# Performance work log

Measured on AMD Instinct MI355X. Metric: run time of the kernel, lower is better.

Reference implementation:

```python
import jax, jax.numpy as jnp
import numpy as np

NUM_USER = 100000
NUM_ITEM = 50000
DIM = 64
NUM_EDGES = 3200000


def setup_inputs() -> dict:
    key = jax.random.key(0)
    k1, k2, k3, k4 = jax.random.split(key, 4)
    return {
        "user_embedding": jax.random.normal(k1, (NUM_USER, DIM), dtype=jnp.float32),
        "item_embedding": jax.random.normal(k2, (NUM_ITEM, DIM), dtype=jnp.float32),
        "edge_user": jax.random.randint(k3, (NUM_EDGES,), 0, NUM_USER, dtype=jnp.int32).astype(jnp.int64),
        "edge_item": jax.random.randint(k4, (NUM_EDGES,), 0, NUM_ITEM, dtype=jnp.int32).astype(jnp.int64),
    }


def _segment_mean(feats, idx, num_segments):
    # scatter_mean semantics: sum per segment / count, empty segments -> 0
    s = jax.ops.segment_sum(feats, idx, num_segments=num_segments)  # [n, dim]
    cnt = jax.ops.segment_sum(jnp.ones((idx.shape[0], 1), feats.dtype), idx,
                              num_segments=num_segments)  # [n, 1]
    return s / jnp.maximum(cnt, 1.0)


def reference(user_embedding, item_embedding, edge_user, edge_item):
    num_user = user_embedding.shape[0]
    num_item = item_embedding.shape[0]

    # view1: aggregate_neighbor_features — mean of purchased-item embeddings per user
    neighbor_feat = _segment_mean(item_embedding[edge_item], edge_user, num_user)

    # view2: aggregate_cooccurrence_features — two-stage mean aggregation
    # stage 1: per item, mean of its purchasers' embeddings
    item_user_agg = _segment_mean(user_embedding[edge_user], edge_item, num_item)
    # stage 2: per user, mean of stage-1 features of purchased items
    cooccur_feat = _segment_mean(item_user_agg[edge_item], edge_user, num_user)

    return (neighbor_feat, cooccur_feat)
```

## Files before the change

### kernel.cpp

```cpp
#include <hip/hip_runtime.h>
#include <hip/hip_fp16.h>

constexpr int NUM_USER  = 100000;
constexpr int NUM_ITEM  = 50000;
constexpr int DIM       = 64;
constexpr int NUM_EDGES = 3200000;

constexpr int KPB   = 32;
constexpr int NB_U  = (NUM_USER + KPB - 1) / KPB;
constexpr int NB_I  = (NUM_ITEM + KPB - 1) / KPB;
constexpr int CHUNK = 4096;
constexpr int CSH   = 14;
constexpr int NCH_I = 4;
constexpr int NCH_U = 7;
constexpr int CAP_U = 1280;
constexpr int CAP_I = 2304;
constexpr int PGRID = 256;
constexpr int CVTB  = 256;
constexpr int NG    = 196;
constexpr int GSH_U = 9;
constexpr int GSH_I = 8;
constexpr int FBG_U = 16;
constexpr int FBG_I = 8;
constexpr int GCAP  = 17152;

__device__ __forceinline__ __half2 u2h(unsigned u) {
  union { unsigned u; __half2 h; } v; v.u = u; return v.h;
}
__device__ __forceinline__ unsigned h2u(__half2 h) {
  union { __half2 h; unsigned u; } v; v.h = h; return v.u;
}
__device__ __forceinline__ float u_as_f(unsigned u) {
  union { unsigned u; float f; } v; v.u = u; return v.f;
}

__device__ __forceinline__ int detect64(const void* eu, const void* ei) {
  const int* a = (const int*)eu;
  const int* b = (const int*)ei;
  int any = 0;
#pragma unroll
  for (int i = 1; i < 64; i += 2) { any |= a[i]; any |= b[i]; }
  return any == 0;
}

__device__ __forceinline__ int idx_at(const void* p, int e, int is64) {
  return is64 ? ((const int*)p)[2 * e] : ((const int*)p)[e];
}

__device__ __forceinline__ void cvt_body(int t0, int stride,
                                         const float* __restrict__ ue,
                                         unsigned* __restrict__ u32,
                                         const float* __restrict__ ie,
                                         unsigned* __restrict__ fused) {
  const int nu = NUM_USER * 32, ni = NUM_ITEM * 32;
  for (int t = t0; t < nu + ni; t += stride) {
    if (t < nu) {
      const unsigned long long raw =
          __builtin_nontemporal_load((const unsigned long long*)ue + t);
      const __half2 h = __floats2half2_rn(u_as_f((unsigned)raw),
                                          u_as_f((unsigned)(raw >> 32)));
      __builtin_nontemporal_store(h2u(h), &u32[t]);
    } else {
      const int s = t - nu;
      const unsigned long long raw =
          __builtin_nontemporal_load((const unsigned long long*)ie + s);
      const __half2 h = __floats2half2_rn(u_as_f((unsigned)raw),
                                          u_as_f((unsigned)(raw >> 32)));
      __builtin_nontemporal_store(h2u(h),
                                  &fused[(size_t)(s >> 5) * 64 + 2 * (s & 31)]);
    }
  }
}

__global__ void k_passA(const void* eu_p, const void* ei_p,
                        int* gccur_u, int* gccur_i,
                        unsigned* __restrict__ coarse_u,
                        unsigned* __restrict__ coarse_i,
                        const float* __restrict__ ue, unsigned* __restrict__ u32t,
                        const float* __restrict__ ie, unsigned* __restrict__ fusedt) {
  __shared__ int hu[NG], bu[NG];
  __shared__ int hi_[NG], bi_[NG];
  if (blockIdx.x >= PGRID) {
    cvt_body((blockIdx.x - PGRID) * blockDim.x + threadIdx.x,
             CVTB * blockDim.x, ue, u32t, ie, fusedt);
    return;
  }
  for (int t = threadIdx.x; t < NG; t += blockDim.x) { hu[t] = 0; hi_[t] = 0; }
  __syncthreads();
  const int is64 = detect64(eu_p, ei_p);
  const int ch = NUM_EDGES / PGRID;
  const int lo = blockIdx.x * ch, hiE = lo + ch;
  for (int e = lo + threadIdx.x; e < hiE; e += blockDim.x) {
    atomicAdd(&hu[idx_at(eu_p, e, is64) >> GSH_U], 1);
    atomicAdd(&hi_[idx_at(ei_p, e, is64) >> GSH_I], 1);
  }
  __syncthreads();
  for (int t = threadIdx.x; t < NG; t += blockDim.x) {
    const int h0 = hu[t];
    bu[t] = h0 ? atomicAdd(&gccur_u[t], h0) : 0;
    hu[t] = 0;
    const int h1 = hi_[t];
    bi_[t] = h1 ? atomicAdd(&gccur_i[t], h1) : 0;
    hi_[t] = 0;
  }
  __syncthreads();
  for (int e = lo + threadIdx.x; e < hiE; e += blockDim.x) {
    const int eu = idx_at(eu_p, e, is64);
    const int ei = idx_at(ei_p, e, is64);
    const int gu = eu >> GSH_U;
    const int pu = bu[gu] + atomicAdd(&hu[gu], 1);
    if (pu < GCAP)
      coarse_u[(size_t)gu * GCAP + pu] =
          ((unsigned)(eu & ((1 << GSH_U) - 1)) << 17) | (unsigned)ei;
    const int gi = ei >> GSH_I;
    const int pi = bi_[gi] + atomicAdd(&hi_[gi], 1);
    if (pi < GCAP)
      coarse_i[(size_t)gi * GCAP + pi] =
          ((unsigned)(ei & ((1 << GSH_I) - 1)) << 17) | (unsigned)eu;
  }
}

__global__ void k_passB(const unsigned* __restrict__ coarse_u,
                        const unsigned* __restrict__ coarse_i,
                        const int* __restrict__ gccur_u,
                        const int* __restrict__ gccur_i,
                        unsigned* __restrict__ pairs_u,
                        unsigned* __restrict__ pairs_i,
                        int* __restrict__ gcnt_u, int* __restrict__ gcnt_i) {
  __shared__ int h[FBG_U], cur[FBG_U];
  const bool isU = blockIdx.x < NG;
  const int g = isU ? blockIdx.x : blockIdx.x - NG;
  const unsigned* src = (isU ? coarse_u : coarse_i) + (size_t)g * GCAP;
  int n = isU ? gccur_u[g] : gccur_i[g];
  n = min(n, GCAP);
  const int FB = isU ? FBG_U : FBG_I;
  const int CAP = isU ? CAP_U : CAP_I;
  const int NBfin = isU ? NB_U : NB_I;
  unsigned* dst = isU ? pairs_u : pairs_i;
  int* gcnt = isU ? gcnt_u : gcnt_i;
  const int tid = threadIdx.x;

  if (tid < FB) h[tid] = 0;
  __syncthreads();
  for (int j = tid; j < n; j += blockDim.x)
    atomicAdd(&h[(src[j] >> 22) & (FB - 1)], 1);
  __syncthreads();
  if (tid < FB) {
    const int fbg = g * FB + tid;
    if (fbg < NBfin) gcnt[fbg] = min(h[tid], CAP);
    cur[tid] = 0;
  }
  __syncthreads();
  for (int j = tid; j < n; j += blockDim.x) {
    const unsigned p = src[j];
    const int fb = (p >> 22) & (FB - 1);
    const int pos = atomicAdd(&cur[fb], 1);
    if (pos < CAP)
      dst[(size_t)(g * FB + fb) * CAP + pos] = p & 0x3FFFFFu;
  }
}

__global__ void k_part2cvt(const void* eu_p, const void* ei_p,
                           int* gcur_i, unsigned int* __restrict__ pairs_i,
                           int* gcur_u, unsigned int* __restrict__ pairs_u,
                           const float* __restrict__ ue, unsigned* __restrict__ u32t,
                           const float* __restrict__ ie, unsigned* __restrict__ fusedt) {
  __shared__ int hist_u[NB_U], base_u[NB_U];
  __shared__ int hist_i[NB_I], base_i[NB_I];
  if (blockIdx.x >= PGRID) {
    cvt_body((blockIdx.x - PGRID) * blockDim.x + threadIdx.x,
             CVTB * blockDim.x, ue, u32t, ie, fusedt);
    return;
  }
  for (int t = threadIdx.x; t < NB_U; t += blockDim.x) hist_u[t] = 0;
  for (int t = threadIdx.x; t < NB_I; t += blockDim.x) hist_i[t] = 0;
  __syncthreads();
  const int is64 = detect64(eu_p, ei_p);
  const int ch = NUM_EDGES / PGRID;
  const int lo = blockIdx.x * ch, hiE = lo + ch;
  for (int e = lo + threadIdx.x; e < hiE; e += blockDim.x) {
    atomicAdd(&hist_u[idx_at(eu_p, e, is64) >> 5], 1);
    atomicAdd(&hist_i[idx_at(ei_p, e, is64) >> 5], 1);
  }
  __syncthreads();
  for (int t = threadIdx.x; t < NB_U; t += blockDim.x) {
    const int h = hist_u[t];
    base_u[t] = h ? t * CAP_U + atomicAdd(&gcur_u[t], h) : 0;
    hist_u[t] = 0;
  }
  for (int t = threadIdx.x; t < NB_I; t += blockDim.x) {
    const int h = hist_i[t];
    base_i[t] = h ? t * CAP_I + atomicAdd(&gcur_i[t], h) : 0;
    hist_i[t] = 0;
  }
  __syncthreads();
  for (int e = lo + threadIdx.x; e < hiE; e += blockDim.x) {
    const int eu = idx_at(eu_p, e, is64);
    const int ei = idx_at(ei_p, e, is64);
    const int bi = ei >> 5;
    const int pi = base_i[bi] + atomicAdd(&hist_i[bi], 1);
    if (pi < (bi + 1) * CAP_I)
      pairs_i[pi] = ((unsigned)(ei & 31) << 17) | (unsigned)eu;
    const int bu = eu >> 5;
    const int pu = base_u[bu] + atomicAdd(&hist_u[bu], 1);
    if (pu < (bu + 1) * CAP_U)
      pairs_u[pu] = ((unsigned)(eu & 31) << 17) | (unsigned)ei;
  }
}

__global__ __launch_bounds__(256, 8)
void k_agg_item(const unsigned* __restrict__ user32,
                const unsigned int* __restrict__ pairs,
                const int* __restrict__ gcnt,
                unsigned* __restrict__ fused) {
  constexpr int NBINS = NCH_U * KPB;
  __shared__ int sorted[CHUNK];
  __shared__ int hist[NBINS], base[NBINS], cur[NBINS];
  __shared__ int gsum[NCH_U];
  const int tid = threadIdx.x;
  const int lane = tid & 63;
  const int wid = tid >> 6;
  const int half = lane >> 5;
  const int c = lane & 31;
  const int bucket = blockIdx.x;
  const int lo = bucket * CAP_I;
  const int hi = lo + min(gcnt[bucket], CAP_I);

  unsigned s[8]; int cnt[8];
#pragma unroll
  for (int r = 0; r < 8; ++r) { s[r] = 0u; cnt[r] = 0; }

  for (int clo = lo; clo < hi; clo += CHUNK) {
    const int csz = min(CHUNK, hi - clo);
    for (int t = tid; t < NBINS; t += 256) hist[t] = 0;
    __syncthreads();
    for (int j = tid; j < csz; j += 256) {
      const unsigned p = pairs[clo + j];
      atomicAdd(&hist[((p & 0x1FFFF) >> CSH) * KPB + (p >> 17)], 1);
    }
    __syncthreads();
    if (tid < NCH_U) {
      int g = 0;
      for (int q = 0; q < KPB; ++q) g += hist[tid * KPB + q];
      gsum[tid] = g;
    }
    __syncthreads();
    for (int t = tid; t < NBINS; t += 256) {
      const int ch = t >> 5;
      int b = 0;
      for (int q = 0; q < ch; ++q) b += gsum[q];
      for (int q = ch * KPB; q < t; ++q) b += hist[q];
      base[t] = b; cur[t] = b;
    }
    __syncthreads();
    for (int j = tid; j < csz; j += 256) {
      const unsigned p = pairs[clo + j];
      const int v = (int)(p & 0x1FFFF);
      const int slot = atomicAdd(&cur[(v >> CSH) * KPB + (p >> 17)], 1);
      sorted[slot] = v;
    }
    __syncthreads();
    for (int ch = 0; ch < NCH_U; ++ch) {
#pragma unroll
      for (int r = 0; r < 8; ++r) {
        const int bin = ch * KPB + wid * 8 + r;
        const int jlo = base[bin], jhi = cur[bin];
        cnt[r] += jhi - jlo;
        for (int j = jlo; j < jhi; j += 8) {
          unsigned w[4];
#pragma unroll
          for (int q = 0; q < 4; ++q) {
            const int jj = j + 2 * q + half;
            w[q] = (jj < jhi) ? user32[(size_t)sorted[jj] * 32 + c] : 0u;
          }
#pragma unroll
          for (int q = 0; q < 4; ++q)
            s[r] = h2u(__hadd2(u2h(s[r]), u2h(w[q])));
        }
      }
    }
    __syncthreads();
  }

  const int i0 = bucket * KPB;
#pragma unroll
  for (int r = 0; r < 8; ++r) {
    const unsigned o = (unsigned)__shfl_xor((int)s[r], 32);
    const __half2 tot = __hadd2(u2h(s[r]), u2h(o));
    const int item = i0 + wid * 8 + r;
    if (half == 0 && item < NUM_ITEM) {
      const float inv = 1.0f / fmaxf((float)cnt[r], 1.f);
      fused[(size_t)item * 64 + 2 * c + 1] =
          h2u(__floats2half2_rn(__low2float(tot) * inv, __high2float(tot) * inv));
    }
  }
}

__global__ __launch_bounds__(256, 8)
void k_agg_user(const unsigned* __restrict__ fused,
                const unsigned int* __restrict__ pairs,
                const int* __restrict__ gcnt,
                float* __restrict__ out0, float* __restrict__ out1) {
  constexpr int NBINS = NCH_I * KPB;
  __shared__ int sorted[CHUNK];
  __shared__ int hist[NBINS], base[NBINS], cur[NBINS];
  __shared__ int gsum[NCH_I];
  const int tid = threadIdx.x;
  const int lane = tid & 63;
  const int wid = tid >> 6;
  const int half = lane >> 5;
  const int c = lane & 31;
  const int bucket = blockIdx.x;
  const int lo = bucket * CAP_U;
  const int hi = lo + min(gcnt[bucket], CAP_U);
  const uint2* fused2 = (const uint2*)fused;

  unsigned s0[8], s1[8]; int cnt[8];
#pragma unroll
  for (int r = 0; r < 8; ++r) { s0[r] = 0u; s1[r] = 0u; cnt[r] = 0; }

  for (int clo = lo; clo < hi; clo += CHUNK) {
    const int csz = min(CHUNK, hi - clo);
    for (int t = tid; t < NBINS; t += 256) hist[t] = 0;
    __syncthreads();
    for (int j = tid; j < csz; j += 256) {
      const unsigned p = pairs[clo + j];
      atomicAdd(&hist[((p & 0x1FFFF) >> CSH) * KPB + (p >> 17)], 1);
    }
    __syncthreads();
    if (tid < NCH_I) {
      int g = 0;
      for (int q = 0; q < KPB; ++q) g += hist[tid * KPB + q];
      gsum[tid] = g;
    }
    __syncthreads();
    for (int t = tid; t < NBINS; t += 256) {
      const int ch = t >> 5;
      int b = 0;
      for (int q = 0; q < ch; ++q) b += gsum[q];
      for (int q = ch * KPB; q < t; ++q) b += hist[q];
      base[t] = b; cur[t] = b;
    }
    __syncthreads();
    for (int j = tid; j < csz; j += 256) {
      const unsigned p = pairs[clo + j];
      const int v = (int)(p & 0x1FFFF);
      const int slot = atomicAdd(&cur[(v >> CSH) * KPB + (p >> 17)], 1);
      sorted[slot] = v;
    }
    __syncthreads();
    for (int ch = 0; ch < NCH_I; ++ch) {
#pragma unroll
      for (int r = 0; r < 8; ++r) {
        const int bin = ch * KPB + wid * 8 + r;
        const int jlo = base[bin], jhi = cur[bin];
        cnt[r] += jhi - jlo;
        for (int j = jlo; j < jhi; j += 8) {
          uint2 w[4];
#pragma unroll
          for (int q = 0; q < 4; ++q) {
            const int jj = j + 2 * q + half;
            w[q] = (jj < jhi) ? fused2[(size_t)sorted[jj] * 32 + c]
                              : make_uint2(0u, 0u);
          }
#pragma unroll
          for (int q = 0; q < 4; ++q) {
            s0[r] = h2u(__hadd2(u2h(s0[r]), u2h(w[q].x)));
            s1[r] = h2u(__hadd2(u2h(s1[r]), u2h(w[q].y)));
          }
        }
      }
    }
    __syncthreads();
  }

  const int u0 = bucket * KPB;
#pragma unroll
  for (int r = 0; r < 8; ++r) {
    const unsigned o0 = (unsigned)__shfl_xor((int)s0[r], 32);
    const unsigned o1 = (unsigned)__shfl_xor((int)s1[r], 32);
    const __half2 t0 = __hadd2(u2h(s0[r]), u2h(o0));
    const __half2 t1 = __hadd2(u2h(s1[r]), u2h(o1));
    const int u = u0 + wid * 8 + r;
    if (half == 0 && u < NUM_USER) {
      const float inv = 1.0f / fmaxf((float)cnt[r], 1.f);
      ((float2*)out0)[(size_t)u * 32 + c] =
          make_float2(__low2float(t0) * inv, __high2float(t0) * inv);
      ((float2*)out1)[(size_t)u * 32 + c] =
          make_float2(__low2float(t1) * inv, __high2float(t1) * inv);
    }
  }
}

__global__ void k_scatter1(const float* __restrict__ user_emb,
                           const float* __restrict__ item_emb,
                           const void* eu_p, const void* ei_p,
                           float* out0, float* item_sum,
                           float* cnt_user, float* cnt_item) {
  const int is64 = detect64(eu_p, ei_p);
  const int lane = threadIdx.x & (DIM - 1);
  const int sub  = threadIdx.x >> 6;
  const int epb  = blockDim.x >> 6;
  for (int e = blockIdx.x * epb + sub; e < NUM_EDGES; e += gridDim.x * epb) {
    const int eu = idx_at(eu_p, e, is64);
    const int ei = idx_at(ei_p, e, is64);
    atomicAdd(&out0[eu * DIM + lane], item_emb[ei * DIM + lane]);
    atomicAdd(&item_sum[ei * DIM + lane], user_emb[eu * DIM + lane]);
    if (lane == 0) {
      atomicAdd(&cnt_user[eu], 1.0f);
      atomicAdd(&cnt_item[ei], 1.0f);
    }
  }
}

__global__ void k_div_item(float* item_sum, const float* __restrict__ cnt_item) {
  const int n = NUM_ITEM * DIM;
  for (int t = blockIdx.x * blockDim.x + threadIdx.x; t < n;
       t += gridDim.x * blockDim.x)
    item_sum[t] /= fmaxf(cnt_item[t >> 6], 1.0f);
}

__global__ void k_scatter2(const float* __restrict__ item_agg,
                           const void* eu_p, const void* ei_p, float* out1) {
  const int is64 = detect64(eu_p, ei_p);
  const int lane = threadIdx.x & (DIM - 1);
  const int sub  = threadIdx.x >> 6;
  const int epb  = blockDim.x >> 6;
  for (int e = blockIdx.x * epb + sub; e < NUM_EDGES; e += gridDim.x * epb) {
    const int eu = idx_at(eu_p, e, is64);
    const int ei = idx_at(ei_p, e, is64);
    atomicAdd(&out1[eu * DIM + lane], item_agg[ei * DIM + lane]);
  }
}

__global__ void k_finalize(float* out0, float* out1,
                           const float* __restrict__ cnt_user) {
  const int n = NUM_USER * DIM;
  for (int t = blockIdx.x * blockDim.x + threadIdx.x; t < n;
       t += gridDim.x * blockDim.x) {
    const float c = fmaxf(cnt_user[t >> 6], 1.0f);
    out0[t] /= c;
    out1[t] /= c;
  }
}

extern "C" void kernel_launch(void* const* d_in, const int* in_sizes, int n_in,
                              void* d_out, int out_size, void* d_ws, size_t ws_size,
                              hipStream_t stream) {
  const float* user_emb = (const float*)d_in[0];
  const float* item_emb = (const float*)d_in[1];
  const void*  eu_p     = d_in[2];
  const void*  ei_p     = d_in[3];

  float* out0 = (float*)d_out;
  float* out1 = out0 + (size_t)NUM_USER * DIM;

  int* wsi = (int*)d_ws;
  float* wsf = (float*)d_ws;

  const size_t t0_coarse_u = 0;
  const size_t t0_coarse_i = t0_coarse_u + (size_t)NG * GCAP;
  const size_t t0_pairs_u  = t0_coarse_i + (size_t)NG * GCAP;
  const size_t t0_pairs_i  = t0_pairs_u + (size_t)NB_U * CAP_U;
  const size_t t0_user32   = t0_pairs_i + (size_t)NB_I * CAP_I;
  const size_t t0_fused    = t0_user32 + (size_t)NUM_USER * 32;
  const size_t t0_gccur    = t0_fused + (size_t)NUM_ITEM * 64;
  const size_t t0_gcnt_u   = t0_gccur + 2 * NG;
  const size_t t0_gcnt_i   = t0_gcnt_u + NB_U;
  const size_t need_t0     = (t0_gcnt_i + NB_I) * 4;

  const size_t s_pairs_u = 0;
  const size_t s_pairs_i = s_pairs_u + (size_t)NB_U * CAP_U;
  const size_t s_user32  = s_pairs_i + (size_t)NB_I * CAP_I;
  const size_t s_fused   = s_user32 + (size_t)NUM_USER * 32;
  const size_t s_gcur_u  = s_fused + (size_t)NUM_ITEM * 64;
  const size_t s_gcur_i  = s_gcur_u + NB_U;
  const size_t need_t1   = (s_gcur_i + NB_I) * 4;

  if (ws_size >= need_t0) {
    unsigned* coarse_u = (unsigned*)(wsi + t0_coarse_u);
    unsigned* coarse_i = (unsigned*)(wsi + t0_coarse_i);
    unsigned* pairs_u  = (unsigned*)(wsi + t0_pairs_u);
    unsigned* pairs_i  = (unsigned*)(wsi + t0_pairs_i);
    unsigned* user32   = (unsigned*)(wsi + t0_user32);
    unsigned* fused    = (unsigned*)(wsi + t0_fused);
    int* gccur_u = wsi + t0_gccur;
    int* gccur_i = gccur_u + NG;
    int* gcnt_u  = wsi + t0_gcnt_u;
    int* gcnt_i  = wsi + t0_gcnt_i;

    hipMemsetAsync(gccur_u, 0, (size_t)(2 * NG) * 4, stream);
    k_passA<<<PGRID + CVTB, 1024, 0, stream>>>(eu_p, ei_p, gccur_u, gccur_i,
                                               coarse_u, coarse_i,
                                               user_emb, user32, item_emb, fused);
    k_passB<<<2 * NG, 1024, 0, stream>>>(coarse_u, coarse_i, gccur_u, gccur_i,
                                         pairs_u, pairs_i, gcnt_u, gcnt_i);
    k_agg_item<<<NB_I, 256, 0, stream>>>(user32, pairs_i, gcnt_i, fused);
    k_agg_user<<<NB_U, 256, 0, stream>>>(fused, pairs_u, gcnt_u, out0, out1);
  } else if (ws_size >= need_t1) {
    unsigned* pairs_u = (unsigned*)(wsi + s_pairs_u);
    unsigned* pairs_i = (unsigned*)(wsi + s_pairs_i);
    unsigned* user32  = (unsigned*)(wsi + s_user32);
    unsigned* fused   = (unsigned*)(wsi + s_fused);
    int* gcur_u = wsi + s_gcur_u;
    int* gcur_i = wsi + s_gcur_i;

    hipMemsetAsync(gcur_u, 0, (size_t)(NB_U + NB_I) * 4, stream);
    k_part2cvt<<<PGRID + CVTB, 1024, 0, stream>>>(eu_p, ei_p, gcur_i, pairs_i,
                                                  gcur_u, pairs_u,
                                                  user_emb, user32,
                                                  item_emb, fused);
    k_agg_item<<<NB_I, 256, 0, stream>>>(user32, pairs_i, gcur_i, fused);
    k_agg_user<<<NB_U, 256, 0, stream>>>(fused, pairs_u, gcur_u, out0, out1);
  } else {
    float* item_sum = wsf;
    float* cnt_user = wsf + (size_t)NUM_ITEM * DIM;
    float* cnt_item = cnt_user + NUM_USER;
    const size_t used = ((size_t)NUM_ITEM * DIM + NUM_USER + NUM_ITEM) * 4;

    hipMemsetAsync(d_out, 0, (size_t)out_size * sizeof(float), stream);
    hipMemsetAsync(d_ws, 0, used, stream);
    k_scatter1<<<4096, 256, 0, stream>>>(user_emb, item_emb, eu_p, ei_p,
                                         out0, item_sum, cnt_user, cnt_item);
    k_div_item<<<2048, 256, 0, stream>>>(item_sum, cnt_item);
    k_scatter2<<<4096, 256, 0, stream>>>(item_sum, eu_p, ei_p, out1);
    k_finalize<<<2048, 256, 0, stream>>>(out0, out1, cnt_user);
  }
}
```

Baseline: 227.8 us.

## Sort pairs by fine bin in passB and drop per-block re-sort in aggregators

passB now builds a full histogram over (fine bucket, chunk, key) bins, computes exclusive prefix offsets, writes pairs in fully sorted order, and stores per-bin offsets as 16-bit arrays in workspace. New aggregation kernels read these offsets into shared memory and walk the pre-sorted pairs directly, skipping the per-block shared-memory histogram, scan and scatter. The cost is larger shared histograms and more scan work in passB, plus extra workspace for the offset tables. The aggregators also lose their large shared arrays, which may allow more blocks per CU.

```diff
diff --git a/kernel.cpp b/kernel.cpp
--- a/kernel.cpp
+++ b/kernel.cpp
@@ -13,6 +13,8 @@
 constexpr int CSH   = 14;
 constexpr int NCH_I = 4;
 constexpr int NCH_U = 7;
+constexpr int BPB_U = NCH_I * KPB;
+constexpr int BPB_I = NCH_U * KPB;
 constexpr int CAP_U = 1280;
 constexpr int CAP_I = 2304;
 constexpr int PGRID = 256;
@@ -126,37 +128,205 @@
                         const int* __restrict__ gccur_i,
                         unsigned* __restrict__ pairs_u,
                         unsigned* __restrict__ pairs_i,
-                        int* __restrict__ gcnt_u, int* __restrict__ gcnt_i) {
-  __shared__ int h[FBG_U], cur[FBG_U];
+                        int* __restrict__ gcnt_u, int* __restrict__ gcnt_i,
+                        unsigned short* __restrict__ boff_u,
+                        unsigned short* __restrict__ boff_i) {
+  __shared__ int hist[FBG_U * BPB_U];
+  __shared__ int base[FBG_U * BPB_U];
+  __shared__ int ssum[FBG_U * (BPB_I / 16)];
+  __shared__ int totl[FBG_U];
   const bool isU = blockIdx.x < NG;
   const int g = isU ? blockIdx.x : blockIdx.x - NG;
   const unsigned* src = (isU ? coarse_u : coarse_i) + (size_t)g * GCAP;
   int n = isU ? gccur_u[g] : gccur_i[g];
   n = min(n, GCAP);
   const int FB = isU ? FBG_U : FBG_I;
+  const int BPB = isU ? BPB_U : BPB_I;
+  const int SEC = BPB >> 4;
   const int CAP = isU ? CAP_U : CAP_I;
   const int NBfin = isU ? NB_U : NB_I;
   unsigned* dst = isU ? pairs_u : pairs_i;
   int* gcnt = isU ? gcnt_u : gcnt_i;
+  unsigned short* boff = isU ? boff_u : boff_i;
+  const int nbins = FB * BPB;
   const int tid = threadIdx.x;
 
-  if (tid < FB) h[tid] = 0;
-  __syncthreads();
-  for (int j = tid; j < n; j += blockDim.x)
-    atomicAdd(&h[(src[j] >> 22) & (FB - 1)], 1);
-  __syncthreads();
-  if (tid < FB) {
-    const int fbg = g * FB + tid;
-    if (fbg < NBfin) gcnt[fbg] = min(h[tid], CAP);
-    cur[tid] = 0;
-  }
+  for (int t = tid; t < nbins; t += blockDim.x) hist[t] = 0;
   __syncthreads();
   for (int j = tid; j < n; j += blockDim.x) {
     const unsigned p = src[j];
-    const int fb = (p >> 22) & (FB - 1);
-    const int pos = atomicAdd(&cur[fb], 1);
+    const int lk = (int)(p >> 17);
+    const int v = (int)(p & 0x1FFFF);
+    atomicAdd(&hist[(lk >> 5) * BPB + (v >> CSH) * KPB + (lk & 31)], 1);
+  }
+  __syncthreads();
+  for (int s = tid; s < FB * SEC; s += blockDim.x) {
+    int acc = 0;
+    const int b0 = s * 16;
+#pragma unroll
+    for (int q = 0; q < 16; ++q) acc += hist[b0 + q];
+    ssum[s] = acc;
+  }
+  __syncthreads();
+  if (tid < FB) {
+    int run = 0;
+    for (int q = 0; q < SEC; ++q) {
+      const int t = ssum[tid * SEC + q];
+      ssum[tid * SEC + q] = run;
+      run += t;
+    }
+    totl[tid] = run;
+  }
+  __syncthreads();
+  for (int b = tid; b < nbins; b += blockDim.x) {
+    const int fb = b / BPB;
+    const int w = b - fb * BPB;
+    const int sec = w >> 4;
+    int acc = ssum[fb * SEC + sec];
+    const int b0 = fb * BPB + (sec << 4);
+    for (int q = b0; q < b; ++q) acc += hist[q];
+    base[b] = acc;
+  }
+  __syncthreads();
+  for (int b = tid; b < nbins; b += blockDim.x) {
+    const int fb = b / BPB;
+    const int fbg = g * FB + fb;
+    if (fbg < NBfin) {
+      const int w = b - fb * BPB;
+      boff[(size_t)fbg * (BPB + 1) + w] = (unsigned short)min(base[b], CAP);
+      if (w == 0) {
+        boff[(size_t)fbg * (BPB + 1) + BPB] = (unsigned short)min(totl[fb], CAP);
+        gcnt[fbg] = min(totl[fb], CAP);
+      }
+    }
+  }
+  __syncthreads();
+  for (int j = tid; j < n; j += blockDim.x) {
+    const unsigned p = src[j];
+    const int lk = (int)(p >> 17);
+    const int v = (int)(p & 0x1FFFF);
+    const int fb = lk >> 5;
+    const int pos = atomicAdd(&base[fb * BPB + (v >> CSH) * KPB + (lk & 31)], 1);
     if (pos < CAP)
-      dst[(size_t)(g * FB + fb) * CAP + pos] = p & 0x3FFFFFu;
+      dst[(size_t)(g * FB + fb) * CAP + pos] = (unsigned)v;
+  }
+}
+
+__global__ __launch_bounds__(256, 8)
+void k_agg_item_f(const unsigned* __restrict__ user32,
+                  const unsigned* __restrict__ pairs,
+                  const unsigned short* __restrict__ boff,
+                  unsigned* __restrict__ fused) {
+  __shared__ unsigned short off[BPB_I + 1];
+  const int tid = threadIdx.x;
+  const int lane = tid & 63;
+  const int wid = tid >> 6;
+  const int half = lane >> 5;
+  const int c = lane & 31;
+  const int bucket = blockIdx.x;
+  for (int t = tid; t < BPB_I + 1; t += 256)
+    off[t] = boff[(size_t)bucket * (BPB_I + 1) + t];
+  __syncthreads();
+  const size_t pbase = (size_t)bucket * CAP_I;
+
+  unsigned s[8]; int cnt[8];
+#pragma unroll
+  for (int r = 0; r < 8; ++r) { s[r] = 0u; cnt[r] = 0; }
+
+  for (int ch = 0; ch < NCH_U; ++ch) {
+#pragma unroll
+    for (int r = 0; r < 8; ++r) {
+      const int bin = ch * KPB + wid * 8 + r;
+      const int jlo = off[bin], jhi = off[bin + 1];
+      cnt[r] += jhi - jlo;
+      for (int j = jlo; j < jhi; j += 8) {
+        unsigned w[4];
+#pragma unroll
+        for (int q = 0; q < 4; ++q) {
+          const int jj = j + 2 * q + half;
+          w[q] = (jj < jhi) ? user32[(size_t)pairs[pbase + jj] * 32 + c] : 0u;
+        }
+#pragma unroll
+        for (int q = 0; q < 4; ++q)
+          s[r] = h2u(__hadd2(u2h(s[r]), u2h(w[q])));
+      }
+    }
+  }
+
+  const int i0 = bucket * KPB;
+#pragma unroll
+  for (int r = 0; r < 8; ++r) {
+    const unsigned o = (unsigned)__shfl_xor((int)s[r], 32);
+    const __half2 tot = __hadd2(u2h(s[r]), u2h(o));
+    const int item = i0 + wid * 8 + r;
+    if (half == 0 && item < NUM_ITEM) {
+      const float inv = 1.0f / fmaxf((float)cnt[r], 1.f);
+      fused[(size_t)item * 64 + 2 * c + 1] =
+          h2u(__floats2half2_rn(__low2float(tot) * inv, __high2float(tot) * inv));
+    }
+  }
+}
+
+__global__ __launch_bounds__(256, 8)
+void k_agg_user_f(const unsigned* __restrict__ fused,
+                  const unsigned* __restrict__ pairs,
+                  const unsigned short* __restrict__ boff,
+                  float* __restrict__ out0, float* __restrict__ out1) {
+  __shared__ unsigned short off[BPB_U + 1];
+  const int tid = threadIdx.x;
+  const int lane = tid & 63;
+  const int wid = tid >> 6;
+  const int half = lane >> 5;
+  const int c = lane & 31;
+  const int bucket = blockIdx.x;
+  for (int t = tid; t < BPB_U + 1; t += 256)
+    off[t] = boff[(size_t)bucket * (BPB_U + 1) + t];
+  __syncthreads();
+  const size_t pbase = (size_t)bucket * CAP_U;
+  const uint2* fused2 = (const uint2*)fused;
+
+  unsigned s0[8], s1[8]; int cnt[8];
+#pragma unroll
+  for (int r = 0; r < 8; ++r) { s0[r] = 0u; s1[r] = 0u; cnt[r] = 0; }
+
+  for (int ch = 0; ch < NCH_I; ++ch) {
+#pragma unroll
+    for (int r = 0; r < 8; ++r) {
+      const int bin = ch * KPB + wid * 8 + r;
+      const int jlo = off[bin], jhi = off[bin + 1];
+      cnt[r] += jhi - jlo;
+      for (int j = jlo; j < jhi; j += 8) {
+        uint2 w[4];
+#pragma unroll
+        for (int q = 0; q < 4; ++q) {
+          const int jj = j + 2 * q + half;
+          w[q] = (jj < jhi) ? fused2[(size_t)pairs[pbase + jj] * 32 + c]
+                            : make_uint2(0u, 0u);
+        }
+#pragma unroll
+        for (int q = 0; q < 4; ++q) {
+          s0[r] = h2u(__hadd2(u2h(s0[r]), u2h(w[q].x)));
+          s1[r] = h2u(__hadd2(u2h(s1[r]), u2h(w[q].y)));
+        }
+      }
+    }
+  }
+
+  const int u0 = bucket * KPB;
+#pragma unroll
+  for (int r = 0; r < 8; ++r) {
+    const unsigned o0 = (unsigned)__shfl_xor((int)s0[r], 32);
+    const unsigned o1 = (unsigned)__shfl_xor((int)s1[r], 32);
+    const __half2 t0 = __hadd2(u2h(s0[r]), u2h(o0));
+    const __half2 t1 = __hadd2(u2h(s1[r]), u2h(o1));
+    const int u = u0 + wid * 8 + r;
+    if (half == 0 && u < NUM_USER) {
+      const float inv = 1.0f / fmaxf((float)cnt[r], 1.f);
+      ((float2*)out0)[(size_t)u * 32 + c] =
+          make_float2(__low2float(t0) * inv, __high2float(t0) * inv);
+      ((float2*)out1)[(size_t)u * 32 + c] =
+          make_float2(__low2float(t1) * inv, __high2float(t1) * inv);
+    }
   }
 }
 
@@ -209,11 +379,11 @@
 }
 
 __global__ __launch_bounds__(256, 8)
-void k_agg_item(const unsigned* __restrict__ user32,
-                const unsigned int* __restrict__ pairs,
-                const int* __restrict__ gcnt,
-                unsigned* __restrict__ fused) {
-  constexpr int NBINS = NCH_U * KPB;
+void k_agg_item_s(const unsigned* __restrict__ user32,
+                  const unsigned int* __restrict__ pairs,
+                  const int* __restrict__ gcnt,
+                  unsigned* __restrict__ fused) {
+  constexpr int NBINS = BPB_I;
   __shared__ int sorted[CHUNK];
   __shared__ int hist[NBINS], base[NBINS], cur[NBINS];
   __shared__ int gsum[NCH_U];
@@ -225,11 +395,9 @@
   const int bucket = blockIdx.x;
   const int lo = bucket * CAP_I;
   const int hi = lo + min(gcnt[bucket], CAP_I);
-
   unsigned s[8]; int cnt[8];
 #pragma unroll
   for (int r = 0; r < 8; ++r) { s[r] = 0u; cnt[r] = 0; }
-
   for (int clo = lo; clo < hi; clo += CHUNK) {
     const int csz = min(CHUNK, hi - clo);
     for (int t = tid; t < NBINS; t += 256) hist[t] = 0;
@@ -281,7 +449,6 @@
     }
     __syncthreads();
   }
-
   const int i0 = bucket * KPB;
 #pragma unroll
   for (int r = 0; r < 8; ++r) {
@@ -297,11 +464,11 @@
 }
 
 __global__ __launch_bounds__(256, 8)
-void k_agg_user(const unsigned* __restrict__ fused,
-                const unsigned int* __restrict__ pairs,
-                const int* __restrict__ gcnt,
-                float* __restrict__ out0, float* __restrict__ out1) {
-  constexpr int NBINS = NCH_I * KPB;
+void k_agg_user_s(const unsigned* __restrict__ fused,
+                  const unsigned int* __restrict__ pairs,
+                  const int* __restrict__ gcnt,
+                  float* __restrict__ out0, float* __restrict__ out1) {
+  constexpr int NBINS = BPB_U;
   __shared__ int sorted[CHUNK];
   __shared__ int hist[NBINS], base[NBINS], cur[NBINS];
   __shared__ int gsum[NCH_I];
@@ -314,11 +481,9 @@
   const int lo = bucket * CAP_U;
   const int hi = lo + min(gcnt[bucket], CAP_U);
   const uint2* fused2 = (const uint2*)fused;
-
   unsigned s0[8], s1[8]; int cnt[8];
 #pragma unroll
   for (int r = 0; r < 8; ++r) { s0[r] = 0u; s1[r] = 0u; cnt[r] = 0; }
-
   for (int clo = lo; clo < hi; clo += CHUNK) {
     const int csz = min(CHUNK, hi - clo);
     for (int t = tid; t < NBINS; t += 256) hist[t] = 0;
@@ -373,7 +538,6 @@
     }
     __syncthreads();
   }
-
   const int u0 = bucket * KPB;
 #pragma unroll
   for (int r = 0; r < 8; ++r) {
@@ -467,7 +631,11 @@
   const size_t t0_gccur    = t0_fused + (size_t)NUM_ITEM * 64;
   const size_t t0_gcnt_u   = t0_gccur + 2 * NG;
   const size_t t0_gcnt_i   = t0_gcnt_u + NB_U;
-  const size_t need_t0     = (t0_gcnt_i + NB_I) * 4;
+  const size_t t0_boff_u   = t0_gcnt_i + NB_I;
+  const size_t t0_boff_u_w = ((size_t)NB_U * (BPB_U + 1) + 1) / 2;
+  const size_t t0_boff_i   = t0_boff_u + t0_boff_u_w;
+  const size_t t0_boff_i_w = ((size_t)NB_I * (BPB_I + 1) + 1) / 2;
+  const size_t need_t0     = (t0_boff_i + t0_boff_i_w) * 4;
 
   const size_t s_pairs_u = 0;
   const size_t s_pairs_i = s_pairs_u + (size_t)NB_U * CAP_U;
@@ -488,15 +656,18 @@
     int* gccur_i = gccur_u + NG;
     int* gcnt_u  = wsi + t0_gcnt_u;
     int* gcnt_i  = wsi + t0_gcnt_i;
+    unsigned short* boff_u = (unsigned short*)(wsi + t0_boff_u);
+    unsigned short* boff_i = (unsigned short*)(wsi + t0_boff_i);
 
     hipMemsetAsync(gccur_u, 0, (size_t)(2 * NG) * 4, stream);
     k_passA<<<PGRID + CVTB, 1024, 0, stream>>>(eu_p, ei_p, gccur_u, gccur_i,
                                                coarse_u, coarse_i,
                                                user_emb, user32, item_emb, fused);
     k_passB<<<2 * NG, 1024, 0, stream>>>(coarse_u, coarse_i, gccur_u, gccur_i,
-                                         pairs_u, pairs_i, gcnt_u, gcnt_i);
-    k_agg_item<<<NB_I, 256, 0, stream>>>(user32, pairs_i, gcnt_i, fused);
-    k_agg_user<<<NB_U, 256, 0, stream>>>(fused, pairs_u, gcnt_u, out0, out1);
+                                         pairs_u, pairs_i, gcnt_u, gcnt_i,
+                                         boff_u, boff_i);
+    k_agg_item_f<<<NB_I, 256, 0, stream>>>(user32, pairs_i, boff_i, fused);
+    k_agg_user_f<<<NB_U, 256, 0, stream>>>(fused, pairs_u, boff_u, out0, out1);
   } else if (ws_size >= need_t1) {
     unsigned* pairs_u = (unsigned*)(wsi + s_pairs_u);
     unsigned* pairs_i = (unsigned*)(wsi + s_pairs_i);
@@ -510,8 +681,8 @@
                                                   gcur_u, pairs_u,
                                                   user_emb, user32,
                                                   item_emb, fused);
-    k_agg_item<<<NB_I, 256, 0, stream>>>(user32, pairs_i, gcur_i, fused);
-    k_agg_user<<<NB_U, 256, 0, stream>>>(fused, pairs_u, gcur_u, out0, out1);
+    k_agg_item_s<<<NB_I, 256, 0, stream>>>(user32, pairs_i, gcur_i, fused);
+    k_agg_user_s<<<NB_U, 256, 0, stream>>>(fused, pairs_u, gcur_u, out0, out1);
   } else {
     float* item_sum = wsf;
     float* cnt_user = wsf + (size_t)NUM_ITEM * DIM;
```

Measured after the change: 373.2 us. +63.8%, slower.
